# Performance work log

Hardware: AMD Instinct MI355X
Metric: run time of the kernel (lower is better)

The kernel has to match this reference:

```python
import jax, jax.numpy as jnp
import numpy as np

B, T = 64, 256
XD, X2S, HD, ZD, Z2S, QZ, PZ = 128, 256, 512, 64, 256, 256, 256


def setup_inputs() -> dict:
    key = jax.random.key(0)
    ks = iter(jax.random.split(key, 48))

    def w(shape):
        return jax.random.normal(next(ks), shape, dtype=jnp.float32) * 0.02

    def b(shape):
        return jnp.zeros(shape, jnp.float32)

    return dict(
        inputs=jax.random.normal(next(ks), (B, T, XD), dtype=jnp.float32),
        eps=jax.random.normal(next(ks), (B, T, ZD), dtype=jnp.float32),
        # X_transform (two relu Dense)
        Wx1=w((XD, X2S)), bx1=b(X2S), Wx2=w((X2S, X2S)), bx2=b(X2S),
        # Z_transform
        Wz1=w((ZD, Z2S)), bz1=b(Z2S), Wz2=w((Z2S, Z2S)), bz2=b(Z2S),
        # phi encoder (input: concat[x2s, h])
        Wp1=w((X2S + HD, QZ)), bp1=b(QZ), Wp2=w((QZ, QZ)), bp2=b(QZ),
        Wpmu=w((QZ, ZD)), bpmu=b(ZD), Wpsig=w((QZ, ZD)), bpsig=b(ZD),
        # prior (input: h)
        Wr1=w((HD, PZ)), br1=b(PZ), Wr2=w((PZ, PZ)), br2=b(PZ),
        Wrmu=w((PZ, ZD)), brmu=b(ZD), Wrsig=w((PZ, ZD)), brsig=b(ZD),
        # theta decoder (input: concat[z2s, h])
        Wt1=w((Z2S + HD, PZ)), bt1=b(PZ), Wt2=w((PZ, PZ)), bt2=b(PZ),
        Wtmu=w((PZ, XD)), btmu=b(XD), Wtsig=w((PZ, XD)), btsig=b(XD),
        # GRU1 (used for states 1-3, as in source) and GRU2 (state 4).
        # Keras GRUCell reset_after=True: bias has shape [2, 3h].
        k1=w((X2S + Z2S, 3 * HD)), rk1=w((HD, 3 * HD)), b1=b((2, 3 * HD)),
        k2=w((HD, 3 * HD)), rk2=w((HD, 3 * HD)), b2=b((2, 3 * HD)),
    )


def _gru(x, h, k, rk, bias):
    # Keras GRUCell math, reset_after=True, tanh/sigmoid activations.
    mx = x @ k + bias[0]
    mh = h @ rk + bias[1]
    xz, xr, xh = jnp.split(mx, 3, axis=-1)
    hz, hr, hh = jnp.split(mh, 3, axis=-1)
    z = jax.nn.sigmoid(xz + hz)
    r = jax.nn.sigmoid(xr + hr)
    hhat = jnp.tanh(xh + r * hh)
    return z * h + (1.0 - z) * hhat


def _mlp2(x, W1, c1, W2, c2):
    return jax.nn.relu(jax.nn.relu(x @ W1 + c1) @ W2 + c2)


def reference(inputs, eps, Wx1, bx1, Wx2, bx2, Wz1, bz1, Wz2, bz2,
              Wp1, bp1, Wp2, bp2, Wpmu, bpmu, Wpsig, bpsig,
              Wr1, br1, Wr2, br2, Wrmu, brmu, Wrsig, brsig,
              Wt1, bt1, Wt2, bt2, Wtmu, btmu, Wtsig, btsig,
              k1, rk1, b1, k2, rk2, b2):
    batch = inputs.shape[0]
    hd = rk1.shape[0]
    X = _mlp2(inputs, Wx1, bx1, Wx2, bx2)  # [B,T,X2S]

    def step(carry, xs):
        h1, h2, h3, h4 = carry
        x_t, e_t = xs
        phi = _mlp2(jnp.concatenate([x_t, h4], axis=-1), Wp1, bp1, Wp2, bp2)
        pmu = phi @ Wpmu + bpmu
        psig = jax.nn.softplus(phi @ Wpsig + bpsig)
        pr = _mlp2(h4, Wr1, br1, Wr2, br2)
        rmu = pr @ Wrmu + brmu
        rsig = jax.nn.softplus(pr @ Wrsig + brsig)
        z_t = pmu + psig * e_t
        zp = _mlp2(z_t, Wz1, bz1, Wz2, bz2)
        rin = jnp.concatenate([x_t, zp], axis=-1)
        # Source bug kept: GRU1 weights drive states 1-3; GRU2 consumes o1=s1.
        s1 = _gru(rin, h1, k1, rk1, b1)
        s2 = _gru(rin, h2, k1, rk1, b1)
        s3 = _gru(rin, h3, k1, rk1, b1)
        s4 = _gru(s1, h4, k2, rk2, b2)
        return (s1, s2, s3, s4), (s4, pmu, psig, rmu, rsig, zp, z_t)

    h0 = tuple(jnp.zeros((batch, hd), inputs.dtype) for _ in range(4))
    xs = (jnp.swapaxes(X, 0, 1), jnp.swapaxes(eps, 0, 1))  # time-major
    _, ys = jax.lax.scan(step, h0, xs)
    S, pmu, psig, rmu, rsig, zp, z = (jnp.swapaxes(a, 0, 1) for a in ys)
    th = _mlp2(jnp.concatenate([zp, S], axis=-1), Wt1, bt1, Wt2, bt2)
    theta_mu = th @ Wtmu + btmu
    theta_sig = jax.nn.softplus(th @ Wtsig + btsig)
    return theta_mu, theta_sig, z
```

## Files before the change

kernel.cpp:

```cpp
#include <hip/hip_runtime.h>
#include <stdint.h>

#define B_ 64
#define T_ 256
#define XD_ 128
#define X2S_ 256
#define HD_ 512
#define ZD_ 64
#define G3_ 1536

typedef unsigned short bf16u;
typedef __attribute__((ext_vector_type(8))) short short8;
typedef __attribute__((ext_vector_type(4))) float f32x4;

__device__ inline f32x4 MFMA(short8 a, short8 b, f32x4 c){
  return __builtin_amdgcn_mfma_f32_16x16x32_bf16(a, b, c, 0, 0, 0);
}
__device__ inline bf16u f2bf(float f){
  unsigned int u = __float_as_uint(f);
  u = u + 0x7FFFu + ((u >> 16) & 1u);
  return (bf16u)(u >> 16);
}
__device__ inline float bf2f(bf16u h){ return __uint_as_float(((unsigned int)h) << 16); }
__device__ inline float sigmoidf_(float x){ return 1.0f / (1.0f + expf(-x)); }
__device__ inline float softplusf_(float x){ return fmaxf(x, 0.0f) + log1pf(expf(-fabsf(x))); }

__device__ inline short8 wfrag(const bf16u* Wp, int K, int nt, int kc, int lane){
  return *(const short8*)(Wp + (((size_t)nt * (K >> 5) + kc) * 64 + lane) * 8);
}
__device__ inline short8 afrag_g(const bf16u* A, int rowstride, int m0, int kc, int lane){
  return *(const short8*)(A + (size_t)(m0 + (lane & 15)) * rowstride + kc * 32 + ((lane >> 4) << 3));
}
__device__ inline short8 afrag_l(const char* buf, int KB, int kc, int lane){
  int row = lane & 15;
  int kb  = kc * 64 + ((lane >> 4) << 4);
  return *(const short8*)(buf + row * KB + (kb ^ ((row & 7) << 4)));
}
__device__ inline void lds_store_bf(char* buf, int KB, int row, int col, bf16u v){
  int byte = col * 2;
  *(bf16u*)(buf + row * KB + (byte ^ ((row & 7) << 4))) = v;
}

__global__ void pack_w(const float* __restrict__ src, bf16u* __restrict__ dst, int K, int N){
  int lane = threadIdx.x;
  int idx  = blockIdx.x;
  int KC = K >> 5;
  int nt = idx / KC, kc = idx - nt * KC;
  int col = nt * 16 + (lane & 15);
  int k0  = kc * 32 + ((lane >> 4) << 3);
  short8 v;
#pragma unroll
  for (int j = 0; j < 8; ++j) v[j] = (short)f2bf(src[(size_t)(k0 + j) * N + col]);
  *(short8*)(dst + ((size_t)idx * 64 + lane) * 8) = v;
}

__global__ void cvt_bf(const float* __restrict__ src, bf16u* __restrict__ dst, int n){
  int i = blockIdx.x * 256 + threadIdx.x;
  if (i < n) dst[i] = f2bf(src[i]);
}

template<int ACT, int STORE>
__global__ __launch_bounds__(256)
void gemm_big(const bf16u* __restrict__ A1, int K1,
              const bf16u* __restrict__ A2, int K2,
              const bf16u* __restrict__ Wp,
              const float* __restrict__ bias,
              bf16u* __restrict__ outb, int N){
  int lane = threadIdx.x & 63, wave = threadIdx.x >> 6;
  int m0 = blockIdx.x * 64 + wave * 16;
  int K = K1 + K2;
  int nt0 = blockIdx.y * 4;
  for (int ntl = 0; ntl < 4; ++ntl){
    int nt = nt0 + ntl;
    f32x4 acc = {0.f, 0.f, 0.f, 0.f};
    int KC1 = K1 >> 5;
    for (int kc = 0; kc < KC1; ++kc)
      acc = MFMA(afrag_g(A1, K1, m0, kc, lane), wfrag(Wp, K, nt, kc, lane), acc);
    if (A2){
      int KC2 = K2 >> 5;
      for (int kc = 0; kc < KC2; ++kc)
        acc = MFMA(afrag_g(A2, K2, m0, kc, lane), wfrag(Wp, K, nt, KC1 + kc, lane), acc);
    }
#pragma unroll
    for (int r = 0; r < 4; ++r){
      int row = m0 + ((lane >> 4) << 2) + r;
      int col = nt * 16 + (lane & 15);
      float v = acc[r] + (bias ? bias[col] : 0.f);
      if (ACT == 1) v = fmaxf(v, 0.f);
      if (STORE == 0){
        outb[(size_t)row * N + col] = f2bf(v);
      } else {
        int b = row >> 8, t = row & 255;
        outb[(size_t)(t * 64 + b) * N + col] = f2bf(v);
      }
    }
  }
}

__global__ __launch_bounds__(256)
void gemm_heads(const bf16u* __restrict__ A,
                const bf16u* __restrict__ Wmu, const bf16u* __restrict__ Wsig,
                const float* __restrict__ bmu, const float* __restrict__ bsig,
                float* __restrict__ out_mu, float* __restrict__ out_sig){
  int lane = threadIdx.x & 63, wave = threadIdx.x >> 6;
  int m0 = blockIdx.x * 64 + wave * 16;
  int nt0 = blockIdx.y * 4;
  for (int ntl = 0; ntl < 4; ++ntl){
    int nt = nt0 + ntl;
    f32x4 am = {0.f,0.f,0.f,0.f}, as = {0.f,0.f,0.f,0.f};
    for (int kc = 0; kc < 8; ++kc){
      short8 a = afrag_g(A, 256, m0, kc, lane);
      am = MFMA(a, wfrag(Wmu, 256, nt, kc, lane), am);
      as = MFMA(a, wfrag(Wsig, 256, nt, kc, lane), as);
    }
#pragma unroll
    for (int r = 0; r < 4; ++r){
      int row = m0 + ((lane >> 4) << 2) + r;
      int col = nt * 16 + (lane & 15);
      int b = row & 63, t = row >> 6;
      size_t o = (size_t)(b * 256 + t) * 128 + col;
      out_mu[o]  = am[r] + bmu[col];
      out_sig[o] = softplusf_(as[r] + bsig[col]);
    }
  }
}

struct Ctx {
  const bf16u *Wp1t, *Wp1b, *Wp2, *Wpmu, *Wpsig, *Wz1, *Wz2, *k1t, *k1b, *rk1, *k2, *rk2;
  const float *bp1, *bp2, *bpmu, *bpsig, *bz1, *bz2, *b1, *b2, *eps;
  const bf16u *X2t;
  bf16u *zp_all, *S_all, *h1b, *h4b;
  float *h1f, *h4f, *mh1, *mh4, *out_z;
};

__global__ __launch_bounds__(256)
void k_step_A(Ctx c, int t){
  __shared__ __align__(16) char A0[16 * 1024];
  __shared__ __align__(16) char A1s[16 * 512];
  __shared__ __align__(16) char A2s[16 * 512];
  __shared__ __align__(16) char A3s[16 * 128];
  int lane = threadIdx.x & 63, wave = threadIdx.x >> 6;
  if (blockIdx.x < 4){
    int b0 = blockIdx.x * 16;
    const bf16u* X2row = c.X2t + (size_t)t * 64 * 256;
    for (int i = threadIdx.x; i < 1024; i += 256){
      int r = i >> 6, ch = i & 63;
      *(short8*)(A0 + r * 1024 + ((ch * 16) ^ ((r & 7) << 4))) =
          *(const short8*)(c.h4b + (size_t)(b0 + r) * 512 + ch * 8);
    }
    __syncthreads();
    for (int nt = wave; nt < 16; nt += 4){
      f32x4 acc = {0.f,0.f,0.f,0.f};
#pragma unroll
      for (int kc = 0; kc < 8; ++kc)
        acc = MFMA(afrag_g(X2row, 256, b0, kc, lane), wfrag(c.Wp1t, 256, nt, kc, lane), acc);
#pragma unroll
      for (int kc = 0; kc < 16; ++kc)
        acc = MFMA(afrag_l(A0, 1024, kc, lane), wfrag(c.Wp1b, 512, nt, kc, lane), acc);
#pragma unroll
      for (int r = 0; r < 4; ++r){
        int row = ((lane >> 4) << 2) + r, col = nt * 16 + (lane & 15);
        lds_store_bf(A1s, 512, row, col, f2bf(fmaxf(acc[r] + c.bp1[col], 0.f)));
      }
    }
    __syncthreads();
    for (int nt = wave; nt < 16; nt += 4){
      f32x4 acc = {0.f,0.f,0.f,0.f};
#pragma unroll
      for (int kc = 0; kc < 8; ++kc)
        acc = MFMA(afrag_l(A1s, 512, kc, lane), wfrag(c.Wp2, 256, nt, kc, lane), acc);
#pragma unroll
      for (int r = 0; r < 4; ++r){
        int row = ((lane >> 4) << 2) + r, col = nt * 16 + (lane & 15);
        lds_store_bf(A2s, 512, row, col, f2bf(fmaxf(acc[r] + c.bp2[col], 0.f)));
      }
    }
    __syncthreads();
    {
      int nt = wave;
      f32x4 am = {0.f,0.f,0.f,0.f}, as = {0.f,0.f,0.f,0.f};
#pragma unroll
      for (int kc = 0; kc < 8; ++kc){
        short8 a = afrag_l(A2s, 512, kc, lane);
        am = MFMA(a, wfrag(c.Wpmu, 256, nt, kc, lane), am);
        as = MFMA(a, wfrag(c.Wpsig, 256, nt, kc, lane), as);
      }
#pragma unroll
      for (int r = 0; r < 4; ++r){
        int row = ((lane >> 4) << 2) + r, col = nt * 16 + (lane & 15);
        float mu = am[r] + c.bpmu[col];
        float sg = softplusf_(as[r] + c.bpsig[col]);
        int b = b0 + row;
        float e = c.eps[((size_t)b * 256 + t) * 64 + col];
        float z = mu + sg * e;
        c.out_z[((size_t)b * 256 + t) * 64 + col] = z;
        lds_store_bf(A3s, 128, row, col, f2bf(z));
      }
    }
    __syncthreads();
    for (int nt = wave; nt < 16; nt += 4){
      f32x4 acc = {0.f,0.f,0.f,0.f};
#pragma unroll
      for (int kc = 0; kc < 2; ++kc)
        acc = MFMA(afrag_l(A3s, 128, kc, lane), wfrag(c.Wz1, 64, nt, kc, lane), acc);
#pragma unroll
      for (int r = 0; r < 4; ++r){
        int row = ((lane >> 4) << 2) + r, col = nt * 16 + (lane & 15);
        lds_store_bf(A1s, 512, row, col, f2bf(fmaxf(acc[r] + c.bz1[col], 0.f)));
      }
    }
    __syncthreads();
    for (int nt = wave; nt < 16; nt += 4){
      f32x4 acc = {0.f,0.f,0.f,0.f};
#pragma unroll
      for (int kc = 0; kc < 8; ++kc)
        acc = MFMA(afrag_l(A1s, 512, kc, lane), wfrag(c.Wz2, 256, nt, kc, lane), acc);
#pragma unroll
      for (int r = 0; r < 4; ++r){
        int row = ((lane >> 4) << 2) + r, col = nt * 16 + (lane & 15);
        c.zp_all[(size_t)(t * 64 + b0 + row) * 256 + col] = f2bf(fmaxf(acc[r] + c.bz2[col], 0.f));
      }
    }
  } else {
    int wg = blockIdx.x - 4;
    int j0 = wg * 32;
    int m0 = wave * 16;
    const f32x4 Z4 = {0.f,0.f,0.f,0.f};
    f32x4 acc[6];
#pragma unroll
    for (int i = 0; i < 6; ++i) acc[i] = Z4;
    for (int kc = 0; kc < 16; ++kc){
      short8 a = afrag_g(c.h1b, 512, m0, kc, lane);
#pragma unroll
      for (int g = 0; g < 3; ++g)
#pragma unroll
        for (int i = 0; i < 2; ++i){
          int nt = g * 32 + wg * 2 + i;
          acc[g * 2 + i] = MFMA(a, wfrag(c.rk1, 512, nt, kc, lane), acc[g * 2 + i]);
        }
    }
#pragma unroll
    for (int g = 0; g < 3; ++g)
#pragma unroll
      for (int i = 0; i < 2; ++i)
#pragma unroll
        for (int r = 0; r < 4; ++r){
          int row = m0 + ((lane >> 4) << 2) + r;
          int col = g * 512 + j0 + i * 16 + (lane & 15);
          c.mh1[(size_t)row * 1536 + col] = acc[g * 2 + i][r] + c.b1[1536 + col];
        }
#pragma unroll
    for (int i = 0; i < 6; ++i) acc[i] = Z4;
    for (int kc = 0; kc < 16; ++kc){
      short8 a = afrag_g(c.h4b, 512, m0, kc, lane);
#pragma unroll
      for (int g = 0; g < 3; ++g)
#pragma unroll
        for (int i = 0; i < 2; ++i){
          int nt = g * 32 + wg * 2 + i;
          acc[g * 2 + i] = MFMA(a, wfrag(c.rk2, 512, nt, kc, lane), acc[g * 2 + i]);
        }
    }
#pragma unroll
    for (int g = 0; g < 3; ++g)
#pragma unroll
      for (int i = 0; i < 2; ++i)
#pragma unroll
        for (int r = 0; r < 4; ++r){
          int row = m0 + ((lane >> 4) << 2) + r;
          int col = g * 512 + j0 + i * 16 + (lane & 15);
          c.mh4[(size_t)row * 1536 + col] = acc[g * 2 + i][r] + c.b2[1536 + col];
        }
  }
}

__global__ __launch_bounds__(256)
void k_step_B(Ctx c, int t){
  int lane = threadIdx.x & 63, wave = threadIdx.x >> 6;
  int wg = blockIdx.x, j0 = wg * 32, m0 = wave * 16;
  const f32x4 Z4 = {0.f,0.f,0.f,0.f};
  f32x4 acc[6];
#pragma unroll
  for (int i = 0; i < 6; ++i) acc[i] = Z4;
  const bf16u* X2row = c.X2t + (size_t)t * 64 * 256;
  const bf16u* zprow = c.zp_all + (size_t)t * 64 * 256;
  for (int kc = 0; kc < 8; ++kc){
    short8 a = afrag_g(X2row, 256, m0, kc, lane);
#pragma unroll
    for (int g = 0; g < 3; ++g)
#pragma unroll
      for (int i = 0; i < 2; ++i){
        int nt = g * 32 + wg * 2 + i;
        acc[g * 2 + i] = MFMA(a, wfrag(c.k1t, 256, nt, kc, lane), acc[g * 2 + i]);
      }
  }
  for (int kc = 0; kc < 8; ++kc){
    short8 a = afrag_g(zprow, 256, m0, kc, lane);
#pragma unroll
    for (int g = 0; g < 3; ++g)
#pragma unroll
      for (int i = 0; i < 2; ++i){
        int nt = g * 32 + wg * 2 + i;
        acc[g * 2 + i] = MFMA(a, wfrag(c.k1b, 256, nt, kc, lane), acc[g * 2 + i]);
      }
  }
#pragma unroll
  for (int i = 0; i < 2; ++i)
#pragma unroll
    for (int r = 0; r < 4; ++r){
      int row = m0 + ((lane >> 4) << 2) + r;
      int j = j0 + i * 16 + (lane & 15);
      float xz = acc[0 + i][r] + c.b1[j];
      float xr = acc[2 + i][r] + c.b1[512 + j];
      float xh = acc[4 + i][r] + c.b1[1024 + j];
      float hz = c.mh1[(size_t)row * 1536 + j];
      float hr = c.mh1[(size_t)row * 1536 + 512 + j];
      float hh = c.mh1[(size_t)row * 1536 + 1024 + j];
      float ho = c.h1f[(size_t)row * 512 + j];
      float zg = sigmoidf_(xz + hz);
      float rg = sigmoidf_(xr + hr);
      float hc = tanhf(xh + rg * hh);
      float hn = zg * ho + (1.f - zg) * hc;
      c.h1f[(size_t)row * 512 + j] = hn;
      c.h1b[(size_t)row * 512 + j] = f2bf(hn);
    }
}

__global__ __launch_bounds__(256)
void k_step_C(Ctx c, int t){
  int lane = threadIdx.x & 63, wave = threadIdx.x >> 6;
  int wg = blockIdx.x, j0 = wg * 32, m0 = wave * 16;
  const f32x4 Z4 = {0.f,0.f,0.f,0.f};
  f32x4 acc[6];
#pragma unroll
  for (int i = 0; i < 6; ++i) acc[i] = Z4;
  for (int kc = 0; kc < 16; ++kc){
    short8 a = afrag_g(c.h1b, 512, m0, kc, lane);
#pragma unroll
    for (int g = 0; g < 3; ++g)
#pragma unroll
      for (int i = 0; i < 2; ++i){
        int nt = g * 32 + wg * 2 + i;
        acc[g * 2 + i] = MFMA(a, wfrag(c.k2, 512, nt, kc, lane), acc[g * 2 + i]);
      }
  }
#pragma unroll
  for (int i = 0; i < 2; ++i)
#pragma unroll
    for (int r = 0; r < 4; ++r){
      int row = m0 + ((lane >> 4) << 2) + r;
      int j = j0 + i * 16 + (lane & 15);
      float xz = acc[0 + i][r] + c.b2[j];
      float xr = acc[2 + i][r] + c.b2[512 + j];
      float xh = acc[4 + i][r] + c.b2[1024 + j];
      float hz = c.mh4[(size_t)row * 1536 + j];
      float hr = c.mh4[(size_t)row * 1536 + 512 + j];
      float hh = c.mh4[(size_t)row * 1536 + 1024 + j];
      float ho = c.h4f[(size_t)row * 512 + j];
      float zg = sigmoidf_(xz + hz);
      float rg = sigmoidf_(xr + hr);
      float hc = tanhf(xh + rg * hh);
      float hn = zg * ho + (1.f - zg) * hc;
      c.h4f[(size_t)row * 512 + j] = hn;
      bf16u hb = f2bf(hn);
      c.h4b[(size_t)row * 512 + j] = hb;
      c.S_all[(size_t)(t * 64 + row) * 512 + j] = hb;
    }
}

extern "C" void kernel_launch(void* const* d_in, const int* in_sizes, int n_in,
                              void* d_out, int out_size, void* d_ws, size_t ws_size,
                              hipStream_t stream){
  const float* inp   = (const float*)d_in[0];
  const float* eps   = (const float*)d_in[1];
  const float* Wx1   = (const float*)d_in[2];  const float* bx1 = (const float*)d_in[3];
  const float* Wx2   = (const float*)d_in[4];  const float* bx2 = (const float*)d_in[5];
  const float* Wz1   = (const float*)d_in[6];  const float* bz1 = (const float*)d_in[7];
  const float* Wz2   = (const float*)d_in[8];  const float* bz2 = (const float*)d_in[9];
  const float* Wp1   = (const float*)d_in[10]; const float* bp1 = (const float*)d_in[11];
  const float* Wp2   = (const float*)d_in[12]; const float* bp2 = (const float*)d_in[13];
  const float* Wpmu  = (const float*)d_in[14]; const float* bpmu = (const float*)d_in[15];
  const float* Wpsig = (const float*)d_in[16]; const float* bpsig = (const float*)d_in[17];
  const float* Wt1   = (const float*)d_in[26]; const float* bt1 = (const float*)d_in[27];
  const float* Wt2   = (const float*)d_in[28]; const float* bt2 = (const float*)d_in[29];
  const float* Wtmu  = (const float*)d_in[30]; const float* btmu = (const float*)d_in[31];
  const float* Wtsig = (const float*)d_in[32]; const float* btsig = (const float*)d_in[33];
  const float* k1    = (const float*)d_in[34];
  const float* rk1   = (const float*)d_in[35];
  const float* b1    = (const float*)d_in[36];
  const float* k2    = (const float*)d_in[37];
  const float* rk2   = (const float*)d_in[38];
  const float* b2    = (const float*)d_in[39];

  float* out_mu  = (float*)d_out;
  float* out_sig = out_mu + (size_t)16384 * 128;
  float* out_z   = out_sig + (size_t)16384 * 128;

  char* p = (char*)d_ws;
  auto alloc = [&](size_t bytes)->char*{ char* r = p; p += (bytes + 255) & ~(size_t)255; return r; };

  bf16u* Wx1p  = (bf16u*)alloc((size_t)128 * 256 * 2);
  bf16u* Wx2p  = (bf16u*)alloc((size_t)256 * 256 * 2);
  bf16u* Wp1t  = (bf16u*)alloc((size_t)256 * 256 * 2);
  bf16u* Wp1b  = (bf16u*)alloc((size_t)512 * 256 * 2);
  bf16u* Wp2p  = (bf16u*)alloc((size_t)256 * 256 * 2);
  bf16u* Wpmup = (bf16u*)alloc((size_t)256 * 64 * 2);
  bf16u* Wpsigp= (bf16u*)alloc((size_t)256 * 64 * 2);
  bf16u* Wz1p  = (bf16u*)alloc((size_t)64 * 256 * 2);
  bf16u* Wz2p  = (bf16u*)alloc((size_t)256 * 256 * 2);
  bf16u* Wt1p  = (bf16u*)alloc((size_t)768 * 256 * 2);
  bf16u* Wt2p  = (bf16u*)alloc((size_t)256 * 256 * 2);
  bf16u* Wtmup = (bf16u*)alloc((size_t)256 * 128 * 2);
  bf16u* Wtsigp= (bf16u*)alloc((size_t)256 * 128 * 2);
  bf16u* k1t   = (bf16u*)alloc((size_t)256 * 1536 * 2);
  bf16u* k1b   = (bf16u*)alloc((size_t)256 * 1536 * 2);
  bf16u* rk1p  = (bf16u*)alloc((size_t)512 * 1536 * 2);
  bf16u* k2p   = (bf16u*)alloc((size_t)512 * 1536 * 2);
  bf16u* rk2p  = (bf16u*)alloc((size_t)512 * 1536 * 2);

  bf16u* Xbf    = (bf16u*)alloc((size_t)16384 * 128 * 2);
  bf16u* tmp1   = (bf16u*)alloc((size_t)16384 * 256 * 2);
  bf16u* X2t    = (bf16u*)alloc((size_t)16384 * 256 * 2);
  bf16u* zp_all = (bf16u*)alloc((size_t)16384 * 256 * 2);
  bf16u* S_all  = (bf16u*)alloc((size_t)16384 * 512 * 2);
  float* h1f = (float*)alloc((size_t)64 * 512 * 4);
  float* h4f = (float*)alloc((size_t)64 * 512 * 4);
  bf16u* h1b = (bf16u*)alloc((size_t)64 * 512 * 2);
  bf16u* h4b = (bf16u*)alloc((size_t)64 * 512 * 2);
  float* mh1 = (float*)alloc((size_t)64 * 1536 * 4);
  float* mh4 = (float*)alloc((size_t)64 * 1536 * 4);
  bf16u* th1 = tmp1;
  bf16u* th2 = X2t;

  auto PK = [&](const float* src, bf16u* dst, int K, int N){
    pack_w<<<dim3((N / 16) * (K / 32)), dim3(64), 0, stream>>>(src, dst, K, N);
  };
  PK(Wx1, Wx1p, 128, 256);
  PK(Wx2, Wx2p, 256, 256);
  PK(Wp1, Wp1t, 256, 256);
  PK(Wp1 + (size_t)256 * 256, Wp1b, 512, 256);
  PK(Wp2, Wp2p, 256, 256);
  PK(Wpmu, Wpmup, 256, 64);
  PK(Wpsig, Wpsigp, 256, 64);
  PK(Wz1, Wz1p, 64, 256);
  PK(Wz2, Wz2p, 256, 256);
  PK(Wt1, Wt1p, 768, 256);
  PK(Wt2, Wt2p, 256, 256);
  PK(Wtmu, Wtmup, 256, 128);
  PK(Wtsig, Wtsigp, 256, 128);
  PK(k1, k1t, 256, 1536);
  PK(k1 + (size_t)256 * 1536, k1b, 256, 1536);
  PK(rk1, rk1p, 512, 1536);
  PK(k2, k2p, 512, 1536);
  PK(rk2, rk2p, 512, 1536);

  cvt_bf<<<dim3((16384 * 128 + 255) / 256), dim3(256), 0, stream>>>(inp, Xbf, 16384 * 128);
  hipMemsetAsync(h1f, 0, (size_t)64 * 512 * 4, stream);
  hipMemsetAsync(h4f, 0, (size_t)64 * 512 * 4, stream);
  hipMemsetAsync(h1b, 0, (size_t)64 * 512 * 2, stream);
  hipMemsetAsync(h4b, 0, (size_t)64 * 512 * 2, stream);

  gemm_big<1, 0><<<dim3(256, 4), dim3(256), 0, stream>>>(Xbf, 128, nullptr, 0, Wx1p, bx1, tmp1, 256);
  gemm_big<1, 1><<<dim3(256, 4), dim3(256), 0, stream>>>(tmp1, 256, nullptr, 0, Wx2p, bx2, X2t, 256);

  Ctx c;
  c.Wp1t = Wp1t; c.Wp1b = Wp1b; c.Wp2 = Wp2p; c.Wpmu = Wpmup; c.Wpsig = Wpsigp;
  c.Wz1 = Wz1p; c.Wz2 = Wz2p; c.k1t = k1t; c.k1b = k1b; c.rk1 = rk1p; c.k2 = k2p; c.rk2 = rk2p;
  c.bp1 = bp1; c.bp2 = bp2; c.bpmu = bpmu; c.bpsig = bpsig; c.bz1 = bz1; c.bz2 = bz2;
  c.b1 = b1; c.b2 = b2; c.eps = eps;
  c.X2t = X2t; c.zp_all = zp_all; c.S_all = S_all;
  c.h1b = h1b; c.h4b = h4b; c.h1f = h1f; c.h4f = h4f; c.mh1 = mh1; c.mh4 = mh4;
  c.out_z = out_z;

  for (int t = 0; t < 256; ++t){
    k_step_A<<<dim3(20), dim3(256), 0, stream>>>(c, t);
    k_step_B<<<dim3(16), dim3(256), 0, stream>>>(c, t);
    k_step_C<<<dim3(16), dim3(256), 0, stream>>>(c, t);
  }

  gemm_big<1, 0><<<dim3(256, 4), dim3(256), 0, stream>>>(zp_all, 256, S_all, 512, Wt1p, bt1, th1, 256);
  gemm_big<1, 0><<<dim3(256, 4), dim3(256), 0, stream>>>(th1, 256, nullptr, 0, Wt2p, bt2, th2, 256);
  gemm_heads<<<dim3(256, 2), dim3(256), 0, stream>>>(th2, Wtmup, Wtsigp, btmu, btsig, out_mu, out_sig);
}
```

Baseline: 12.45 ms.

## Replace per-timestep kernel launches with a persistent cooperative scan kernel

Replaces the 768 per-timestep launches (three kernels per step) with one cooperative persistent kernel of 68 workgroups that loops over all 256 timesteps and separates phases with grid-wide syncs. GRU workgroups keep their slices of the recurrent and input weights resident in LDS and hold the fp32 hidden state in registers, which removes the fp32 h buffers and the mh intermediate round-trips through global memory. The recurrent matmul is issued before the first grid sync so it overlaps with the encoder path. The cost is three grid barriers per step, 96KB of LDS per workgroup, and GRU1 and GRU2 now each use only 32 workgroups with 16 units apiece.

```diff
diff --git a/kernel.cpp b/kernel.cpp
--- a/kernel.cpp
+++ b/kernel.cpp
@@ -1,13 +1,8 @@
 #include <hip/hip_runtime.h>
+#include <hip/hip_cooperative_groups.h>
 #include <stdint.h>
 
-#define B_ 64
-#define T_ 256
-#define XD_ 128
-#define X2S_ 256
-#define HD_ 512
-#define ZD_ 64
-#define G3_ 1536
+namespace cg = cooperative_groups;
 
 typedef unsigned short bf16u;
 typedef __attribute__((ext_vector_type(8))) short short8;
@@ -39,6 +34,9 @@
 __device__ inline void lds_store_bf(char* buf, int KB, int row, int col, bf16u v){
   int byte = col * 2;
   *(bf16u*)(buf + row * KB + (byte ^ ((row & 7) << 4))) = v;
+}
+__device__ inline short8 lfrag(const char* slab, int ntl, int kc, int lane){
+  return *(const short8*)(slab + (size_t)(ntl * 16 + kc) * 1024 + lane * 16);
 }
 
 __global__ void pack_w(const float* __restrict__ src, bf16u* __restrict__ dst, int K, int N){
@@ -125,247 +123,223 @@
   }
 }
 
-struct Ctx {
-  const bf16u *Wp1t, *Wp1b, *Wp2, *Wpmu, *Wpsig, *Wz1, *Wz2, *k1t, *k1b, *rk1, *k2, *rk2;
+struct SCtx {
+  const bf16u *Wp1, *Wp2, *Wpmu, *Wpsig, *Wz1, *Wz2;
+  const bf16u *k1, *rk1, *k2, *rk2;
   const float *bp1, *bp2, *bpmu, *bpsig, *bz1, *bz2, *b1, *b2, *eps;
   const bf16u *X2t;
   bf16u *zp_all, *S_all, *h1b, *h4b;
-  float *h1f, *h4f, *mh1, *mh4, *out_z;
+  float *out_z;
 };
 
-__global__ __launch_bounds__(256)
-void k_step_A(Ctx c, int t){
-  __shared__ __align__(16) char A0[16 * 1024];
-  __shared__ __align__(16) char A1s[16 * 512];
-  __shared__ __align__(16) char A2s[16 * 512];
-  __shared__ __align__(16) char A3s[16 * 128];
-  int lane = threadIdx.x & 63, wave = threadIdx.x >> 6;
-  if (blockIdx.x < 4){
-    int b0 = blockIdx.x * 16;
-    const bf16u* X2row = c.X2t + (size_t)t * 64 * 256;
-    for (int i = threadIdx.x; i < 1024; i += 256){
-      int r = i >> 6, ch = i & 63;
-      *(short8*)(A0 + r * 1024 + ((ch * 16) ^ ((r & 7) << 4))) =
-          *(const short8*)(c.h4b + (size_t)(b0 + r) * 512 + ch * 8);
+__global__ __launch_bounds__(256, 1)
+void scan_persist(SCtx c){
+  __shared__ __align__(16) char SLDS[98304];
+  cg::grid_group grid = cg::this_grid();
+  const int lane = threadIdx.x & 63, wave = threadIdx.x >> 6;
+  const int wg = blockIdx.x;
+
+  if (wg < 4){
+    char* A0  = SLDS;
+    char* A1s = SLDS + 16384;
+    char* A2s = SLDS + 24576;
+    char* A3s = SLDS + 32768;
+    const int b0 = wg * 16;
+    for (int t = 0; t < 256; ++t){
+      const bf16u* X2row = c.X2t + (size_t)t * 64 * 256;
+      for (int i = threadIdx.x; i < 1024; i += 256){
+        int r = i >> 6, ch = i & 63;
+        *(short8*)(A0 + r * 1024 + ((ch * 16) ^ ((r & 7) << 4))) =
+            *(const short8*)(c.h4b + (size_t)(b0 + r) * 512 + ch * 8);
+      }
+      __syncthreads();
+      for (int nt = wave; nt < 16; nt += 4){
+        f32x4 acc = {0.f,0.f,0.f,0.f};
+#pragma unroll
+        for (int kc = 0; kc < 8; ++kc)
+          acc = MFMA(afrag_g(X2row, 256, b0, kc, lane), wfrag(c.Wp1, 768, nt, kc, lane), acc);
+#pragma unroll
+        for (int kc = 0; kc < 16; ++kc)
+          acc = MFMA(afrag_l(A0, 1024, kc, lane), wfrag(c.Wp1, 768, nt, 8 + kc, lane), acc);
+#pragma unroll
+        for (int r = 0; r < 4; ++r){
+          int row = ((lane >> 4) << 2) + r, col = nt * 16 + (lane & 15);
+          lds_store_bf(A1s, 512, row, col, f2bf(fmaxf(acc[r] + c.bp1[col], 0.f)));
+        }
+      }
+      __syncthreads();
+      for (int nt = wave; nt < 16; nt += 4){
+        f32x4 acc = {0.f,0.f,0.f,0.f};
+#pragma unroll
+        for (int kc = 0; kc < 8; ++kc)
+          acc = MFMA(afrag_l(A1s, 512, kc, lane), wfrag(c.Wp2, 256, nt, kc, lane), acc);
+#pragma unroll
+        for (int r = 0; r < 4; ++r){
+          int row = ((lane >> 4) << 2) + r, col = nt * 16 + (lane & 15);
+          lds_store_bf(A2s, 512, row, col, f2bf(fmaxf(acc[r] + c.bp2[col], 0.f)));
+        }
+      }
+      __syncthreads();
+      {
+        int nt = wave;
+        f32x4 am = {0.f,0.f,0.f,0.f}, as = {0.f,0.f,0.f,0.f};
+#pragma unroll
+        for (int kc = 0; kc < 8; ++kc){
+          short8 a = afrag_l(A2s, 512, kc, lane);
+          am = MFMA(a, wfrag(c.Wpmu, 256, nt, kc, lane), am);
+          as = MFMA(a, wfrag(c.Wpsig, 256, nt, kc, lane), as);
+        }
+#pragma unroll
+        for (int r = 0; r < 4; ++r){
+          int row = ((lane >> 4) << 2) + r, col = nt * 16 + (lane & 15);
+          float mu = am[r] + c.bpmu[col];
+          float sg = softplusf_(as[r] + c.bpsig[col]);
+          int b = b0 + row;
+          float e = c.eps[((size_t)b * 256 + t) * 64 + col];
+          float z = mu + sg * e;
+          c.out_z[((size_t)b * 256 + t) * 64 + col] = z;
+          lds_store_bf(A3s, 128, row, col, f2bf(z));
+        }
+      }
+      __syncthreads();
+      for (int nt = wave; nt < 16; nt += 4){
+        f32x4 acc = {0.f,0.f,0.f,0.f};
+#pragma unroll
+        for (int kc = 0; kc < 2; ++kc)
+          acc = MFMA(afrag_l(A3s, 128, kc, lane), wfrag(c.Wz1, 64, nt, kc, lane), acc);
+#pragma unroll
+        for (int r = 0; r < 4; ++r){
+          int row = ((lane >> 4) << 2) + r, col = nt * 16 + (lane & 15);
+          lds_store_bf(A1s, 512, row, col, f2bf(fmaxf(acc[r] + c.bz1[col], 0.f)));
+        }
+      }
+      __syncthreads();
+      for (int nt = wave; nt < 16; nt += 4){
+        f32x4 acc = {0.f,0.f,0.f,0.f};
+#pragma unroll
+        for (int kc = 0; kc < 8; ++kc)
+          acc = MFMA(afrag_l(A1s, 512, kc, lane), wfrag(c.Wz2, 256, nt, kc, lane), acc);
+#pragma unroll
+        for (int r = 0; r < 4; ++r){
+          int row = ((lane >> 4) << 2) + r, col = nt * 16 + (lane & 15);
+          c.zp_all[(size_t)(t * 64 + b0 + row) * 256 + col] = f2bf(fmaxf(acc[r] + c.bz2[col], 0.f));
+        }
+      }
+      __syncthreads();
+      grid.sync();
+      grid.sync();
+      grid.sync();
+    }
+  } else {
+    const bool g1 = (wg < 36);
+    const int  ui = g1 ? (wg - 4) : (wg - 36);
+    const int  u0 = ui * 16;
+    const bf16u* rkp = g1 ? c.rk1 : c.rk2;
+    const bf16u* kkp = g1 ? c.k1  : c.k2;
+    const float* bias = g1 ? c.b1 : c.b2;
+    char* RK = SLDS;
+    char* KK = SLDS + 49152;
+#pragma unroll
+    for (int m = 0; m < 2; ++m){
+      const bf16u* src = m ? kkp : rkp;
+      char* dst = m ? KK : RK;
+      for (int g = 0; g < 3; ++g){
+        const char* s = (const char*)src + (size_t)(g * 32 + ui) * 16384;
+        for (int i = threadIdx.x; i < 1024; i += 256)
+          *(float4*)(dst + g * 16384 + i * 16) = *(const float4*)(s + i * 16);
+      }
     }
     __syncthreads();
-    for (int nt = wave; nt < 16; nt += 4){
-      f32x4 acc = {0.f,0.f,0.f,0.f};
-#pragma unroll
-      for (int kc = 0; kc < 8; ++kc)
-        acc = MFMA(afrag_g(X2row, 256, b0, kc, lane), wfrag(c.Wp1t, 256, nt, kc, lane), acc);
-#pragma unroll
-      for (int kc = 0; kc < 16; ++kc)
-        acc = MFMA(afrag_l(A0, 1024, kc, lane), wfrag(c.Wp1b, 512, nt, kc, lane), acc);
-#pragma unroll
-      for (int r = 0; r < 4; ++r){
-        int row = ((lane >> 4) << 2) + r, col = nt * 16 + (lane & 15);
-        lds_store_bf(A1s, 512, row, col, f2bf(fmaxf(acc[r] + c.bp1[col], 0.f)));
-      }
-    }
-    __syncthreads();
-    for (int nt = wave; nt < 16; nt += 4){
-      f32x4 acc = {0.f,0.f,0.f,0.f};
-#pragma unroll
-      for (int kc = 0; kc < 8; ++kc)
-        acc = MFMA(afrag_l(A1s, 512, kc, lane), wfrag(c.Wp2, 256, nt, kc, lane), acc);
-#pragma unroll
-      for (int r = 0; r < 4; ++r){
-        int row = ((lane >> 4) << 2) + r, col = nt * 16 + (lane & 15);
-        lds_store_bf(A2s, 512, row, col, f2bf(fmaxf(acc[r] + c.bp2[col], 0.f)));
-      }
-    }
-    __syncthreads();
-    {
-      int nt = wave;
-      f32x4 am = {0.f,0.f,0.f,0.f}, as = {0.f,0.f,0.f,0.f};
-#pragma unroll
-      for (int kc = 0; kc < 8; ++kc){
-        short8 a = afrag_l(A2s, 512, kc, lane);
-        am = MFMA(a, wfrag(c.Wpmu, 256, nt, kc, lane), am);
-        as = MFMA(a, wfrag(c.Wpsig, 256, nt, kc, lane), as);
-      }
-#pragma unroll
-      for (int r = 0; r < 4; ++r){
-        int row = ((lane >> 4) << 2) + r, col = nt * 16 + (lane & 15);
-        float mu = am[r] + c.bpmu[col];
-        float sg = softplusf_(as[r] + c.bpsig[col]);
-        int b = b0 + row;
-        float e = c.eps[((size_t)b * 256 + t) * 64 + col];
-        float z = mu + sg * e;
-        c.out_z[((size_t)b * 256 + t) * 64 + col] = z;
-        lds_store_bf(A3s, 128, row, col, f2bf(z));
-      }
-    }
-    __syncthreads();
-    for (int nt = wave; nt < 16; nt += 4){
-      f32x4 acc = {0.f,0.f,0.f,0.f};
-#pragma unroll
-      for (int kc = 0; kc < 2; ++kc)
-        acc = MFMA(afrag_l(A3s, 128, kc, lane), wfrag(c.Wz1, 64, nt, kc, lane), acc);
-#pragma unroll
-      for (int r = 0; r < 4; ++r){
-        int row = ((lane >> 4) << 2) + r, col = nt * 16 + (lane & 15);
-        lds_store_bf(A1s, 512, row, col, f2bf(fmaxf(acc[r] + c.bz1[col], 0.f)));
-      }
-    }
-    __syncthreads();
-    for (int nt = wave; nt < 16; nt += 4){
-      f32x4 acc = {0.f,0.f,0.f,0.f};
-#pragma unroll
-      for (int kc = 0; kc < 8; ++kc)
-        acc = MFMA(afrag_l(A1s, 512, kc, lane), wfrag(c.Wz2, 256, nt, kc, lane), acc);
-#pragma unroll
-      for (int r = 0; r < 4; ++r){
-        int row = ((lane >> 4) << 2) + r, col = nt * 16 + (lane & 15);
-        c.zp_all[(size_t)(t * 64 + b0 + row) * 256 + col] = f2bf(fmaxf(acc[r] + c.bz2[col], 0.f));
-      }
-    }
-  } else {
-    int wg = blockIdx.x - 4;
-    int j0 = wg * 32;
-    int m0 = wave * 16;
-    const f32x4 Z4 = {0.f,0.f,0.f,0.f};
-    f32x4 acc[6];
-#pragma unroll
-    for (int i = 0; i < 6; ++i) acc[i] = Z4;
-    for (int kc = 0; kc < 16; ++kc){
-      short8 a = afrag_g(c.h1b, 512, m0, kc, lane);
-#pragma unroll
-      for (int g = 0; g < 3; ++g)
-#pragma unroll
-        for (int i = 0; i < 2; ++i){
-          int nt = g * 32 + wg * 2 + i;
-          acc[g * 2 + i] = MFMA(a, wfrag(c.rk1, 512, nt, kc, lane), acc[g * 2 + i]);
-        }
-    }
-#pragma unroll
-    for (int g = 0; g < 3; ++g)
-#pragma unroll
-      for (int i = 0; i < 2; ++i)
-#pragma unroll
-        for (int r = 0; r < 4; ++r){
-          int row = m0 + ((lane >> 4) << 2) + r;
-          int col = g * 512 + j0 + i * 16 + (lane & 15);
-          c.mh1[(size_t)row * 1536 + col] = acc[g * 2 + i][r] + c.b1[1536 + col];
-        }
-#pragma unroll
-    for (int i = 0; i < 6; ++i) acc[i] = Z4;
-    for (int kc = 0; kc < 16; ++kc){
-      short8 a = afrag_g(c.h4b, 512, m0, kc, lane);
-#pragma unroll
-      for (int g = 0; g < 3; ++g)
-#pragma unroll
-        for (int i = 0; i < 2; ++i){
-          int nt = g * 32 + wg * 2 + i;
-          acc[g * 2 + i] = MFMA(a, wfrag(c.rk2, 512, nt, kc, lane), acc[g * 2 + i]);
-        }
-    }
-#pragma unroll
-    for (int g = 0; g < 3; ++g)
-#pragma unroll
-      for (int i = 0; i < 2; ++i)
-#pragma unroll
-        for (int r = 0; r < 4; ++r){
-          int row = m0 + ((lane >> 4) << 2) + r;
-          int col = g * 512 + j0 + i * 16 + (lane & 15);
-          c.mh4[(size_t)row * 1536 + col] = acc[g * 2 + i][r] + c.b2[1536 + col];
-        }
+
+    const int m0 = wave * 16;
+    f32x4 hreg = {0.f, 0.f, 0.f, 0.f};
+    const f32x4 Z4 = {0.f, 0.f, 0.f, 0.f};
+
+    for (int t = 0; t < 256; ++t){
+      f32x4 mz = Z4, mr = Z4, mh = Z4;
+      {
+        const bf16u* hsrc = g1 ? c.h1b : c.h4b;
+#pragma unroll
+        for (int kc = 0; kc < 16; ++kc){
+          short8 a = afrag_g(hsrc, 512, m0, kc, lane);
+          mz = MFMA(a, lfrag(RK, 0, kc, lane), mz);
+          mr = MFMA(a, lfrag(RK, 1, kc, lane), mr);
+          mh = MFMA(a, lfrag(RK, 2, kc, lane), mh);
+        }
+      }
+      grid.sync();
+      if (g1){
+        f32x4 xz = Z4, xr = Z4, xh = Z4;
+        const bf16u* X2row = c.X2t    + (size_t)t * 64 * 256;
+        const bf16u* zprow = c.zp_all + (size_t)t * 64 * 256;
+#pragma unroll
+        for (int kc = 0; kc < 8; ++kc){
+          short8 a = afrag_g(X2row, 256, m0, kc, lane);
+          xz = MFMA(a, lfrag(KK, 0, kc, lane), xz);
+          xr = MFMA(a, lfrag(KK, 1, kc, lane), xr);
+          xh = MFMA(a, lfrag(KK, 2, kc, lane), xh);
+        }
+#pragma unroll
+        for (int kc = 0; kc < 8; ++kc){
+          short8 a = afrag_g(zprow, 256, m0, kc, lane);
+          xz = MFMA(a, lfrag(KK, 0, 8 + kc, lane), xz);
+          xr = MFMA(a, lfrag(KK, 1, 8 + kc, lane), xr);
+          xh = MFMA(a, lfrag(KK, 2, 8 + kc, lane), xh);
+        }
+#pragma unroll
+        for (int r = 0; r < 4; ++r){
+          int row  = m0 + ((lane >> 4) << 2) + r;
+          int unit = u0 + (lane & 15);
+          float xz_ = xz[r] + bias[unit];
+          float xr_ = xr[r] + bias[512 + unit];
+          float xh_ = xh[r] + bias[1024 + unit];
+          float hz_ = mz[r] + bias[1536 + unit];
+          float hr_ = mr[r] + bias[1536 + 512 + unit];
+          float hh_ = mh[r] + bias[1536 + 1024 + unit];
+          float zg = sigmoidf_(xz_ + hz_);
+          float rg = sigmoidf_(xr_ + hr_);
+          float hc = tanhf(xh_ + rg * hh_);
+          float hn = zg * hreg[r] + (1.f - zg) * hc;
+          hreg[r] = hn;
+          c.h1b[(size_t)row * 512 + unit] = f2bf(hn);
+        }
+        __syncthreads();
+        grid.sync();
+        grid.sync();
+      } else {
+        grid.sync();
+        f32x4 xz = Z4, xr = Z4, xh = Z4;
+#pragma unroll
+        for (int kc = 0; kc < 16; ++kc){
+          short8 a = afrag_g(c.h1b, 512, m0, kc, lane);
+          xz = MFMA(a, lfrag(KK, 0, kc, lane), xz);
+          xr = MFMA(a, lfrag(KK, 1, kc, lane), xr);
+          xh = MFMA(a, lfrag(KK, 2, kc, lane), xh);
+        }
+#pragma unroll
+        for (int r = 0; r < 4; ++r){
+          int row  = m0 + ((lane >> 4) << 2) + r;
+          int unit = u0 + (lane & 15);
+          float xz_ = xz[r] + bias[unit];
+          float xr_ = xr[r] + bias[512 + unit];
+          float xh_ = xh[r] + bias[1024 + unit];
+          float hz_ = mz[r] + bias[1536 + unit];
+          float hr_ = mr[r] + bias[1536 + 512 + unit];
+          float hh_ = mh[r] + bias[1536 + 1024 + unit];
+          float zg = sigmoidf_(xz_ + hz_);
+          float rg = sigmoidf_(xr_ + hr_);
+          float hc = tanhf(xh_ + rg * hh_);
+          float hn = zg * hreg[r] + (1.f - zg) * hc;
+          hreg[r] = hn;
+          bf16u hb = f2bf(hn);
+          c.h4b[(size_t)row * 512 + unit] = hb;
+          c.S_all[(size_t)(t * 64 + row) * 512 + unit] = hb;
+        }
+        __syncthreads();
+        grid.sync();
+      }
+    }
   }
-}
-
-__global__ __launch_bounds__(256)
-void k_step_B(Ctx c, int t){
-  int lane = threadIdx.x & 63, wave = threadIdx.x >> 6;
-  int wg = blockIdx.x, j0 = wg * 32, m0 = wave * 16;
-  const f32x4 Z4 = {0.f,0.f,0.f,0.f};
-  f32x4 acc[6];
-#pragma unroll
-  for (int i = 0; i < 6; ++i) acc[i] = Z4;
-  const bf16u* X2row = c.X2t + (size_t)t * 64 * 256;
-  const bf16u* zprow = c.zp_all + (size_t)t * 64 * 256;
-  for (int kc = 0; kc < 8; ++kc){
-    short8 a = afrag_g(X2row, 256, m0, kc, lane);
-#pragma unroll
-    for (int g = 0; g < 3; ++g)
-#pragma unroll
-      for (int i = 0; i < 2; ++i){
-        int nt = g * 32 + wg * 2 + i;
-        acc[g * 2 + i] = MFMA(a, wfrag(c.k1t, 256, nt, kc, lane), acc[g * 2 + i]);
-      }
-  }
-  for (int kc = 0; kc < 8; ++kc){
-    short8 a = afrag_g(zprow, 256, m0, kc, lane);
-#pragma unroll
-    for (int g = 0; g < 3; ++g)
-#pragma unroll
-      for (int i = 0; i < 2; ++i){
-        int nt = g * 32 + wg * 2 + i;
-        acc[g * 2 + i] = MFMA(a, wfrag(c.k1b, 256, nt, kc, lane), acc[g * 2 + i]);
-      }
-  }
-#pragma unroll
-  for (int i = 0; i < 2; ++i)
-#pragma unroll
-    for (int r = 0; r < 4; ++r){
-      int row = m0 + ((lane >> 4) << 2) + r;
-      int j = j0 + i * 16 + (lane & 15);
-      float xz = acc[0 + i][r] + c.b1[j];
-      float xr = acc[2 + i][r] + c.b1[512 + j];
-      float xh = acc[4 + i][r] + c.b1[1024 + j];
-      float hz = c.mh1[(size_t)row * 1536 + j];
-      float hr = c.mh1[(size_t)row * 1536 + 512 + j];
-      float hh = c.mh1[(size_t)row * 1536 + 1024 + j];
-      float ho = c.h1f[(size_t)row * 512 + j];
-      float zg = sigmoidf_(xz + hz);
-      float rg = sigmoidf_(xr + hr);
-      float hc = tanhf(xh + rg * hh);
-      float hn = zg * ho + (1.f - zg) * hc;
-      c.h1f[(size_t)row * 512 + j] = hn;
-      c.h1b[(size_t)row * 512 + j] = f2bf(hn);
-    }
-}
-
-__global__ __launch_bounds__(256)
-void k_step_C(Ctx c, int t){
-  int lane = threadIdx.x & 63, wave = threadIdx.x >> 6;
-  int wg = blockIdx.x, j0 = wg * 32, m0 = wave * 16;
-  const f32x4 Z4 = {0.f,0.f,0.f,0.f};
-  f32x4 acc[6];
-#pragma unroll
-  for (int i = 0; i < 6; ++i) acc[i] = Z4;
-  for (int kc = 0; kc < 16; ++kc){
-    short8 a = afrag_g(c.h1b, 512, m0, kc, lane);
-#pragma unroll
-    for (int g = 0; g < 3; ++g)
-#pragma unroll
-      for (int i = 0; i < 2; ++i){
-        int nt = g * 32 + wg * 2 + i;
-        acc[g * 2 + i] = MFMA(a, wfrag(c.k2, 512, nt, kc, lane), acc[g * 2 + i]);
-      }
-  }
-#pragma unroll
-  for (int i = 0; i < 2; ++i)
-#pragma unroll
-    for (int r = 0; r < 4; ++r){
-      int row = m0 + ((lane >> 4) << 2) + r;
-      int j = j0 + i * 16 + (lane & 15);
-      float xz = acc[0 + i][r] + c.b2[j];
-      float xr = acc[2 + i][r] + c.b2[512 + j];
-      float xh = acc[4 + i][r] + c.b2[1024 + j];
-      float hz = c.mh4[(size_t)row * 1536 + j];
-      float hr = c.mh4[(size_t)row * 1536 + 512 + j];
-      float hh = c.mh4[(size_t)row * 1536 + 1024 + j];
-      float ho = c.h4f[(size_t)row * 512 + j];
-      float zg = sigmoidf_(xz + hz);
-      float rg = sigmoidf_(xr + hr);
-      float hc = tanhf(xh + rg * hh);
-      float hn = zg * ho + (1.f - zg) * hc;
-      c.h4f[(size_t)row * 512 + j] = hn;
-      bf16u hb = f2bf(hn);
-      c.h4b[(size_t)row * 512 + j] = hb;
-      c.S_all[(size_t)(t * 64 + row) * 512 + j] = hb;
-    }
 }
 
 extern "C" void kernel_launch(void* const* d_in, const int* in_sizes, int n_in,
@@ -401,8 +375,7 @@
 
   bf16u* Wx1p  = (bf16u*)alloc((size_t)128 * 256 * 2);
   bf16u* Wx2p  = (bf16u*)alloc((size_t)256 * 256 * 2);
-  bf16u* Wp1t  = (bf16u*)alloc((size_t)256 * 256 * 2);
-  bf16u* Wp1b  = (bf16u*)alloc((size_t)512 * 256 * 2);
+  bf16u* Wp1p  = (bf16u*)alloc((size_t)768 * 256 * 2);
   bf16u* Wp2p  = (bf16u*)alloc((size_t)256 * 256 * 2);
   bf16u* Wpmup = (bf16u*)alloc((size_t)256 * 64 * 2);
   bf16u* Wpsigp= (bf16u*)alloc((size_t)256 * 64 * 2);
@@ -412,8 +385,7 @@
   bf16u* Wt2p  = (bf16u*)alloc((size_t)256 * 256 * 2);
   bf16u* Wtmup = (bf16u*)alloc((size_t)256 * 128 * 2);
   bf16u* Wtsigp= (bf16u*)alloc((size_t)256 * 128 * 2);
-  bf16u* k1t   = (bf16u*)alloc((size_t)256 * 1536 * 2);
-  bf16u* k1b   = (bf16u*)alloc((size_t)256 * 1536 * 2);
+  bf16u* k1p   = (bf16u*)alloc((size_t)512 * 1536 * 2);
   bf16u* rk1p  = (bf16u*)alloc((size_t)512 * 1536 * 2);
   bf16u* k2p   = (bf16u*)alloc((size_t)512 * 1536 * 2);
   bf16u* rk2p  = (bf16u*)alloc((size_t)512 * 1536 * 2);
@@ -423,12 +395,8 @@
   bf16u* X2t    = (bf16u*)alloc((size_t)16384 * 256 * 2);
   bf16u* zp_all = (bf16u*)alloc((size_t)16384 * 256 * 2);
   bf16u* S_all  = (bf16u*)alloc((size_t)16384 * 512 * 2);
-  float* h1f = (float*)alloc((size_t)64 * 512 * 4);
-  float* h4f = (float*)alloc((size_t)64 * 512 * 4);
-  bf16u* h1b = (bf16u*)alloc((size_t)64 * 512 * 2);
-  bf16u* h4b = (bf16u*)alloc((size_t)64 * 512 * 2);
-  float* mh1 = (float*)alloc((size_t)64 * 1536 * 4);
-  float* mh4 = (float*)alloc((size_t)64 * 1536 * 4);
+  bf16u* h1b    = (bf16u*)alloc((size_t)64 * 512 * 2);
+  bf16u* h4b    = (bf16u*)alloc((size_t)64 * 512 * 2);
   bf16u* th1 = tmp1;
   bf16u* th2 = X2t;
 
@@ -437,8 +405,7 @@
   };
   PK(Wx1, Wx1p, 128, 256);
   PK(Wx2, Wx2p, 256, 256);
-  PK(Wp1, Wp1t, 256, 256);
-  PK(Wp1 + (size_t)256 * 256, Wp1b, 512, 256);
+  PK(Wp1, Wp1p, 768, 256);
   PK(Wp2, Wp2p, 256, 256);
   PK(Wpmu, Wpmup, 256, 64);
   PK(Wpsig, Wpsigp, 256, 64);
@@ -448,35 +415,29 @@
   PK(Wt2, Wt2p, 256, 256);
   PK(Wtmu, Wtmup, 256, 128);
   PK(Wtsig, Wtsigp, 256, 128);
-  PK(k1, k1t, 256, 1536);
-  PK(k1 + (size_t)256 * 1536, k1b, 256, 1536);
+  PK(k1, k1p, 512, 1536);
   PK(rk1, rk1p, 512, 1536);
   PK(k2, k2p, 512, 1536);
   PK(rk2, rk2p, 512, 1536);
 
   cvt_bf<<<dim3((16384 * 128 + 255) / 256), dim3(256), 0, stream>>>(inp, Xbf, 16384 * 128);
-  hipMemsetAsync(h1f, 0, (size_t)64 * 512 * 4, stream);
-  hipMemsetAsync(h4f, 0, (size_t)64 * 512 * 4, stream);
   hipMemsetAsync(h1b, 0, (size_t)64 * 512 * 2, stream);
   hipMemsetAsync(h4b, 0, (size_t)64 * 512 * 2, stream);
 
   gemm_big<1, 0><<<dim3(256, 4), dim3(256), 0, stream>>>(Xbf, 128, nullptr, 0, Wx1p, bx1, tmp1, 256);
   gemm_big<1, 1><<<dim3(256, 4), dim3(256), 0, stream>>>(tmp1, 256, nullptr, 0, Wx2p, bx2, X2t, 256);
 
-  Ctx c;
-  c.Wp1t = Wp1t; c.Wp1b = Wp1b; c.Wp2 = Wp2p; c.Wpmu = Wpmup; c.Wpsig = Wpsigp;
-  c.Wz1 = Wz1p; c.Wz2 = Wz2p; c.k1t = k1t; c.k1b = k1b; c.rk1 = rk1p; c.k2 = k2p; c.rk2 = rk2p;
-  c.bp1 = bp1; c.bp2 = bp2; c.bpmu = bpmu; c.bpsig = bpsig; c.bz1 = bz1; c.bz2 = bz2;
-  c.b1 = b1; c.b2 = b2; c.eps = eps;
-  c.X2t = X2t; c.zp_all = zp_all; c.S_all = S_all;
-  c.h1b = h1b; c.h4b = h4b; c.h1f = h1f; c.h4f = h4f; c.mh1 = mh1; c.mh4 = mh4;
-  c.out_z = out_z;
-
-  for (int t = 0; t < 256; ++t){
-    k_step_A<<<dim3(20), dim3(256), 0, stream>>>(c, t);
-    k_step_B<<<dim3(16), dim3(256), 0, stream>>>(c, t);
-    k_step_C<<<dim3(16), dim3(256), 0, stream>>>(c, t);
-  }
+  SCtx sc;
+  sc.Wp1 = Wp1p; sc.Wp2 = Wp2p; sc.Wpmu = Wpmup; sc.Wpsig = Wpsigp;
+  sc.Wz1 = Wz1p; sc.Wz2 = Wz2p;
+  sc.k1 = k1p; sc.rk1 = rk1p; sc.k2 = k2p; sc.rk2 = rk2p;
+  sc.bp1 = bp1; sc.bp2 = bp2; sc.bpmu = bpmu; sc.bpsig = bpsig;
+  sc.bz1 = bz1; sc.bz2 = bz2; sc.b1 = b1; sc.b2 = b2; sc.eps = eps;
+  sc.X2t = X2t; sc.zp_all = zp_all; sc.S_all = S_all;
+  sc.h1b = h1b; sc.h4b = h4b; sc.out_z = out_z;
+
+  void* args[] = { (void*)&sc };
+  hipLaunchCooperativeKernel((const void*)scan_persist, dim3(68), dim3(256), args, 0, stream);
 
   gemm_big<1, 0><<<dim3(256, 4), dim3(256), 0, stream>>>(zp_all, 256, S_all, 512, Wt1p, bt1, th1, 256);
   gemm_big<1, 0><<<dim3(256, 4), dim3(256), 0, stream>>>(th1, 256, nullptr, 0, Wt2p, bt2, th2, 256);
```

Result: faster. 10.80 ms (-13.3%).
